# Kernel tuning notes

Hardware: AMD Instinct MI355X
Metric: run time of the kernel (lower is better)

The kernel has to match this reference:

```python
import jax, jax.numpy as jnp
import numpy as np

B, S, D, H, E, K, F = 1, 1024, 1024, 16, 8, 2, 4096


def setup_inputs() -> dict:
    key = jax.random.key(0)
    ks = jax.random.split(key, 8)
    n = lambda k, shape, sc: (jax.random.normal(k, shape, dtype=jnp.float32) * sc)
    return {
        "x": n(ks[0], (B, S, D), 1.0),
        "w_qkv": n(ks[1], (D, 3 * D), D ** -0.5),
        "w_o": n(ks[2], (D, D), D ** -0.5),
        "g1": jnp.ones((D,), jnp.float32),
        "b1": jnp.zeros((D,), jnp.float32),
        "wg": n(ks[3], (D, E), D ** -0.5),
        "w1": n(ks[4], (E, D, F), D ** -0.5),
        "bb1": jnp.zeros((E, F), jnp.float32),
        "w2": n(ks[5], (E, F, D), F ** -0.5),
        "bb2": jnp.zeros((E, D), jnp.float32),
        "g2": jnp.ones((D,), jnp.float32),
        "b2": jnp.zeros((D,), jnp.float32),
    }


def layernorm(x, g, b, eps=1e-5):
    m = x.mean(-1, keepdims=True)
    v = ((x - m) ** 2).mean(-1, keepdims=True)
    return (x - m) * jax.lax.rsqrt(v + eps) * g + b


def reference(x, w_qkv, w_o, g1, b1, wg, w1, bb1, w2, bb2, g2, b2):
    b, s, d = x.shape
    hd = d // H
    # --- multi-head causal self-attention ---
    qkv = x @ w_qkv  # [b,s,3d]
    q, k, v = jnp.split(qkv, 3, axis=-1)
    to_heads = lambda t: t.reshape(b, s, H, hd).transpose(0, 2, 1, 3)  # [b,h,s,hd]
    q, k, v = to_heads(q), to_heads(k), to_heads(v)
    scores = jnp.einsum("bhqd,bhkd->bhqk", q, k) / jnp.sqrt(jnp.float32(hd))
    causal = jnp.tril(jnp.ones((s, s), bool))
    scores = jnp.where(causal, scores, jnp.finfo(scores.dtype).min)
    attn = jax.nn.softmax(scores, axis=-1)
    o = jnp.einsum("bhqk,bhkd->bhqd", attn, v)
    o = o.transpose(0, 2, 1, 3).reshape(b, s, d) @ w_o
    # --- add & norm ---
    h = layernorm(x + o, g1, b1)
    # --- MoE FFN: softmax router, top-k, renormalized combine ---
    probs = jax.nn.softmax(h @ wg, axis=-1)  # [b,s,E]
    topv, topi = jax.lax.top_k(probs, K)
    topv = topv / topv.sum(-1, keepdims=True)
    w = (topv[..., None] * jax.nn.one_hot(topi, E, dtype=h.dtype)).sum(-2)  # [b,s,E]
    h1 = jax.nn.gelu(jnp.einsum("bsd,edf->ebsf", h, w1) + bb1[:, None, None, :])
    y = jnp.einsum("ebsf,efd->ebsd", h1, w2) + bb2[:, None, None, :]
    moe = jnp.einsum("ebsd,bse->bsd", y, w)
    # --- residual + norm of MoE block ---
    return layernorm(h + moe, g2, b2)
```

## Files before the change

kernel.cpp:

```cpp
#include <hip/hip_runtime.h>
#include <hip/hip_bf16.h>
#include <math.h>

#define SEQ 1024
#define DIM 1024
#define NH  16
#define NE  8
#define FF  4096
#define NCH 8

typedef float f32x4 __attribute__((ext_vector_type(4)));
typedef float f32x2 __attribute__((ext_vector_type(2)));
typedef short short8 __attribute__((ext_vector_type(8)));
typedef short s16x4 __attribute__((ext_vector_type(4)));

#define WAIT_VM(N) asm volatile("s_waitcnt vmcnt(" #N ")" ::: "memory")

__device__ __forceinline__ ushort f2bf(float f) {
  union { float f; unsigned u; } v; v.f = f;
  unsigned r = v.u + 0x7FFF + ((v.u >> 16) & 1);
  return (ushort)(r >> 16);
}
__device__ __forceinline__ float bf2f(ushort h) {
  union { unsigned u; float f; } v; v.u = ((unsigned)h) << 16;
  return v.f;
}

__device__ __forceinline__ float gelu_tanh(float x) {
  return 0.5f * x * (1.f + tanhf(0.7978845608028654f * (x + 0.044715f * x * x * x)));
}
__device__ __forceinline__ float gelu_fast(float x) {
  float u = 1.5957691216057308f * (x + 0.044715f * x * x * x);
  return x / (1.f + __expf(-u));
}

__device__ __forceinline__ void gl2lds16(const void* g, void* l) {
  __builtin_amdgcn_global_load_lds(
      (const __attribute__((address_space(1))) unsigned int*)g,
      (__attribute__((address_space(3))) unsigned int*)l, 16, 0, 0);
}

__global__ __launch_bounds__(256) void wconv_kernel(
    const float* __restrict__ wq, const float* __restrict__ wo,
    const float* __restrict__ x,
    ushort* __restrict__ wqT, ushort* __restrict__ wqTl,
    ushort* __restrict__ woT, ushort* __restrict__ woTl,
    ushort* __restrict__ xh, ushort* __restrict__ xl) {
  __shared__ __align__(16) ushort th[64 * 64];
  __shared__ __align__(16) ushort tl[64 * 64];
  int z = blockIdx.z, t = threadIdx.x;
  if (z == 2) {
    int blk = blockIdx.y * 64 + blockIdx.x;
    int i = (blk * 256 + t) * 4;
    f32x4 v = *(const f32x4*)&x[i];
    ushort h[4], l[4];
#pragma unroll
    for (int j = 0; j < 4; j++) { h[j] = f2bf(v[j]); l[j] = f2bf(v[j] - bf2f(h[j])); }
    *(s16x4*)&xh[i] = *(const s16x4*)h;
    *(s16x4*)&xl[i] = *(const s16x4*)l;
    return;
  }
  const float* src; ushort* dh; ushort* dl; int R, C, r0, c0;
  if (z == 0) {
    if (blockIdx.x >= 48) return;
    src = wq; dh = wqT; dl = wqTl;
    R = DIM; C = 3 * DIM; r0 = blockIdx.y * 64; c0 = blockIdx.x * 64;
  } else {
    if (blockIdx.x >= 16) return;
    src = wo; dh = woT; dl = woTl;
    R = DIM; C = DIM; r0 = blockIdx.y * 64; c0 = blockIdx.x * 64;
  }
  int ry = (t >> 4) * 4;
  int cx = (t & 15) * 4;
  f32x4 v[4];
#pragma unroll
  for (int j = 0; j < 4; j++)
    v[j] = *(const f32x4*)&src[(size_t)(r0 + ry + j) * C + c0 + cx];
#pragma unroll
  for (int i = 0; i < 4; i++) {
    int trow = cx + i;
    int o = trow * 64 + (((ry >> 3) ^ (trow & 7)) << 3) + (ry & 7);
    ushort uh[4], ul[4];
#pragma unroll
    for (int j = 0; j < 4; j++) {
      float f = v[j][i];
      ushort hh = f2bf(f);
      uh[j] = hh;
      ul[j] = f2bf(f - bf2f(hh));
    }
    *(s16x4*)&th[o] = *(const s16x4*)uh;
    *(s16x4*)&tl[o] = *(const s16x4*)ul;
  }
  __syncthreads();
  int tr = t >> 2, tc = (t & 3) * 16;
  int b0 = (tc >> 3) ^ (tr & 7);
  int b1 = ((tc >> 3) + 1) ^ (tr & 7);
  size_t dbase = (size_t)(c0 + tr) * R + r0 + tc;
  short8 u0 = *(const short8*)&th[tr * 64 + b0 * 8];
  short8 u1 = *(const short8*)&th[tr * 64 + b1 * 8];
  *(short8*)&dh[dbase] = u0;
  *(short8*)&dh[dbase + 8] = u1;
  short8 l0 = *(const short8*)&tl[tr * 64 + b0 * 8];
  short8 l1 = *(const short8*)&tl[tr * 64 + b1 * 8];
  *(short8*)&dl[dbase] = l0;
  *(short8*)&dl[dbase + 8] = l1;
}

__global__ __launch_bounds__(256) void bfsplit_kernel(const float* __restrict__ in,
                                                      ushort* __restrict__ oh,
                                                      ushort* __restrict__ ol) {
  int i = (blockIdx.x * 256 + threadIdx.x) * 4;
  f32x4 v = *(const f32x4*)&in[i];
  ushort h[4], l[4];
#pragma unroll
  for (int j = 0; j < 4; j++) { h[j] = f2bf(v[j]); l[j] = f2bf(v[j] - bf2f(h[j])); }
  *(s16x4*)&oh[i] = *(const s16x4*)h;
  *(s16x4*)&ol[i] = *(const s16x4*)l;
}

#define MM_FEXP_LOAD(ra0v, ra1v, rb0v, rb1v, rb2v, rb3v, T)            \
  { int _ko = (T) * 32;                                                \
    ra0v = *(const short8*)(aG[0] + _ko);                              \
    ra1v = *(const short8*)(aG[1] + _ko);                              \
    rb0v = *(const f32x4*)(bG + (size_t)(_ko + 0) * N);                \
    rb1v = *(const f32x4*)(bG + (size_t)(_ko + 1) * N);                \
    rb2v = *(const f32x4*)(bG + (size_t)(_ko + 2) * N);                \
    rb3v = *(const f32x4*)(bG + (size_t)(_ko + 3) * N); }

#define MM_FEXP_STAGE(buf, ra0v, ra1v, rb0v, rb1v, rb2v, rb3v)         \
  { *(short8*)&As[buf][aw[0]] = ra0v;                                  \
    *(short8*)&As[buf][aw[1]] = ra1v;                                  \
    _Pragma("unroll")                                                  \
    for (int i = 0; i < 4; i++) {                                      \
      ushort u[4];                                                     \
      u[0] = f2bf(rb0v[i]); u[1] = f2bf(rb1v[i]);                      \
      u[2] = f2bf(rb2v[i]); u[3] = f2bf(rb3v[i]);                      \
      *(s16x4*)&Bs[buf][(nb * 4 + i) * 40 + bslot * 4] = *(const s16x4*)u; } }

#define MM_FEXP_MFMA(buf)                                              \
  { short8 af[4], bf[4];                                               \
    _Pragma("unroll")                                                  \
    for (int mi = 0; mi < 4; mi++) af[mi] = *(const short8*)&As[buf][aro[mi]]; \
    _Pragma("unroll")                                                  \
    for (int ni = 0; ni < 4; ni++) bf[ni] = *(const short8*)&Bs[buf][bro[ni]]; \
    _Pragma("unroll")                                                  \
    for (int mi = 0; mi < 4; mi++)                                     \
      _Pragma("unroll")                                                \
      for (int ni = 0; ni < 4; ni++)                                   \
        acc[mi][ni] = __builtin_amdgcn_mfma_f32_16x16x32_bf16(af[mi], bf[ni], acc[mi][ni], 0, 0, 0); }

template <int EPI, int KSPLIT>
__global__ __launch_bounds__(256) void mm_fexp(
    const ushort* __restrict__ A, const float* __restrict__ Bf,
    const float* __restrict__ bias, void* __restrict__ Cout,
    const int* __restrict__ tok, const int* __restrict__ offcnt,
    int N, int K)
{
  int zz = blockIdx.z;
  int e  = (KSPLIT > 1) ? (zz & (NE - 1)) : zz;
  int ks = (KSPLIT > 1) ? (zz >> 3) : 0;
  int off = offcnt[e], cnt = offcnt[NE + e];
  int m0 = blockIdx.y * 128;
  if (m0 >= cnt) return;
  int n0 = blockIdx.x * 128;
  const float* Bp = Bf + (size_t)e * K * N;
  const int Kc = K / KSPLIT, kbase = ks * Kc;

  __shared__ __align__(16) ushort As[2][128 * 32];
  __shared__ __align__(16) ushort Bs[2][128 * 40];

  int t = threadIdx.x, lane = t & 63, w = t >> 6, wr = w >> 1, wc = w & 1;

  const ushort* aG[2]; int aw[2];
#pragma unroll
  for (int c = 0; c < 2; c++) {
    int gid = w * 128 + c * 64 + lane;
    int m = gid >> 2, p = gid & 3;
    int kg = p ^ ((m >> 1) & 3);
    int mc = m0 + m; if (mc > cnt - 1) mc = cnt - 1;
    int arow = tok ? tok[off + mc] : (off + mc);
    aG[c] = A + (size_t)arow * K + kbase + kg * 8;
    aw[c] = gid * 8;
  }

  int kb = t >> 5, nb = t & 31;
  const float* bG = Bp + (size_t)(kbase + kb * 4) * N + n0 + nb * 4;
  int bslot = kb ^ ((nb & 3) << 1);

  int aro[4], bro[4];
#pragma unroll
  for (int mi = 0; mi < 4; mi++) {
    int m = wr * 64 + mi * 16 + (lane & 15);
    aro[mi] = (m * 4 + ((lane >> 4) ^ ((m >> 1) & 3))) * 8;
  }
#pragma unroll
  for (int ni = 0; ni < 4; ni++) {
    int n = wc * 64 + ni * 16 + (lane & 15);
    bro[ni] = n * 40 + ((((lane >> 4) * 2) ^ (((n >> 2) & 3) << 1))) * 4;
  }

  f32x4 acc[4][4] = {};
  const int nt = Kc / 32;

  short8 raA0, raA1, raB0, raB1;
  f32x4 rbA0, rbA1, rbA2, rbA3, rbB0, rbB1, rbB2, rbB3;
  MM_FEXP_LOAD(raA0, raA1, rbA0, rbA1, rbA2, rbA3, 0);
  MM_FEXP_LOAD(raB0, raB1, rbB0, rbB1, rbB2, rbB3, 1);

  for (int tt = 0; tt < nt; tt += 2) {
    MM_FEXP_STAGE(0, raA0, raA1, rbA0, rbA1, rbA2, rbA3);
    if (tt + 2 < nt) MM_FEXP_LOAD(raA0, raA1, rbA0, rbA1, rbA2, rbA3, tt + 2);
    asm volatile("s_waitcnt lgkmcnt(0)" ::: "memory");
    __builtin_amdgcn_sched_barrier(0);
    __builtin_amdgcn_s_barrier();
    MM_FEXP_MFMA(0);
    MM_FEXP_STAGE(1, raB0, raB1, rbB0, rbB1, rbB2, rbB3);
    if (tt + 3 < nt) MM_FEXP_LOAD(raB0, raB1, rbB0, rbB1, rbB2, rbB3, tt + 3);
    asm volatile("s_waitcnt lgkmcnt(0)" ::: "memory");
    __builtin_amdgcn_sched_barrier(0);
    __builtin_amdgcn_s_barrier();
    MM_FEXP_MFMA(1);
  }

  const float* biasp = (EPI == 3) ? nullptr : bias + (size_t)e * N;
  float* Cp = (float*)Cout + (size_t)ks * 2048 * N;
#pragma unroll
  for (int mi = 0; mi < 4; mi++) {
#pragma unroll
    for (int j = 0; j < 4; j++) {
      int grow = m0 + wr * 64 + mi * 16 + (lane >> 4) * 4 + j;
      if (grow >= cnt) continue;
      size_t rbase = (size_t)(off + grow) * N;
#pragma unroll
      for (int ni = 0; ni < 4; ni++) {
        int gcol = n0 + wc * 64 + ni * 16 + (lane & 15);
        float v = acc[mi][ni][j];
        if (EPI == 1) ((ushort*)Cout)[rbase + gcol] = f2bf(gelu_fast(v + biasp[gcol]));
        else          Cp[rbase + gcol] = v;
      }
    }
  }
}

#undef MM_FEXP_LOAD
#undef MM_FEXP_STAGE
#undef MM_FEXP_MFMA

__global__ __launch_bounds__(256) void mm_split(
    const ushort* __restrict__ Ah, const ushort* __restrict__ Al,
    const ushort* __restrict__ Bh, const ushort* __restrict__ Bl,
    float* __restrict__ C, int N, int K)
{
  int m0 = blockIdx.y * 128;
  int n0 = blockIdx.x * 128;

  __shared__ __align__(16) ushort Ahs[2][4096], Als[2][4096];
  __shared__ __align__(16) ushort Bhs[2][4096], Bls[2][4096];

  int t = threadIdx.x, lane = t & 63, w = t >> 6, wr = w >> 1, wc = w & 1;

  const ushort *aGh[2], *aGl[2], *bGh[2], *bGl[2];
  int lofs[2];
#pragma unroll
  for (int c = 0; c < 2; c++) {
    int gid = w * 128 + c * 64 + lane;
    int m = gid >> 2, p = gid & 3;
    int kg = p ^ ((m >> 1) & 3);
    aGh[c] = Ah + (size_t)(m0 + m) * K + kg * 8;
    aGl[c] = Al + (size_t)(m0 + m) * K + kg * 8;
    bGh[c] = Bh + (size_t)(n0 + m) * K + kg * 8;
    bGl[c] = Bl + (size_t)(n0 + m) * K + kg * 8;
    lofs[c] = (w * 128 + c * 64) * 8;
  }

  int aro[4], bro[4];
#pragma unroll
  for (int mi = 0; mi < 4; mi++) {
    int m = wr * 64 + mi * 16 + (lane & 15);
    aro[mi] = (m * 4 + ((lane >> 4) ^ ((m >> 1) & 3))) * 8;
  }
#pragma unroll
  for (int ni = 0; ni < 4; ni++) {
    int n = wc * 64 + ni * 16 + (lane & 15);
    bro[ni] = (n * 4 + ((lane >> 4) ^ ((n >> 1) & 3))) * 8;
  }

  f32x4 acc[4][4] = {};
  const int nt = K / 32;

#pragma unroll
  for (int c = 0; c < 2; c++) {
    gl2lds16(aGh[c], &Ahs[0][lofs[c]]); gl2lds16(aGl[c], &Als[0][lofs[c]]);
    gl2lds16(bGh[c], &Bhs[0][lofs[c]]); gl2lds16(bGl[c], &Bls[0][lofs[c]]);
  }
  if (nt > 1) {
#pragma unroll
    for (int c = 0; c < 2; c++) {
      gl2lds16(aGh[c] + 32, &Ahs[1][lofs[c]]); gl2lds16(aGl[c] + 32, &Als[1][lofs[c]]);
      gl2lds16(bGh[c] + 32, &Bhs[1][lofs[c]]); gl2lds16(bGl[c] + 32, &Bls[1][lofs[c]]);
    }
  }

  for (int tt = 0; tt < nt; tt++) {
    if (tt + 1 < nt) WAIT_VM(8); else WAIT_VM(0);
    __builtin_amdgcn_s_barrier();
    int b = tt & 1;
    short8 ah[4], al_[4], bh[4], bl_[4];
#pragma unroll
    for (int mi = 0; mi < 4; mi++) {
      ah[mi] = *(const short8*)&Ahs[b][aro[mi]];
      al_[mi] = *(const short8*)&Als[b][aro[mi]];
    }
#pragma unroll
    for (int ni = 0; ni < 4; ni++) {
      bh[ni] = *(const short8*)&Bhs[b][bro[ni]];
      bl_[ni] = *(const short8*)&Bls[b][bro[ni]];
    }
#pragma unroll
    for (int mi = 0; mi < 4; mi++)
#pragma unroll
      for (int ni = 0; ni < 4; ni++) {
        acc[mi][ni] = __builtin_amdgcn_mfma_f32_16x16x32_bf16(al_[mi], bh[ni], acc[mi][ni], 0, 0, 0);
        acc[mi][ni] = __builtin_amdgcn_mfma_f32_16x16x32_bf16(ah[mi], bl_[ni], acc[mi][ni], 0, 0, 0);
        acc[mi][ni] = __builtin_amdgcn_mfma_f32_16x16x32_bf16(ah[mi], bh[ni], acc[mi][ni], 0, 0, 0);
      }
    asm volatile("s_waitcnt lgkmcnt(0)" ::: "memory");
    __builtin_amdgcn_sched_barrier(0);
    __builtin_amdgcn_s_barrier();
    if (tt + 2 < nt) {
      int ko = (tt + 2) * 32;
#pragma unroll
      for (int c = 0; c < 2; c++) {
        gl2lds16(aGh[c] + ko, &Ahs[b][lofs[c]]); gl2lds16(aGl[c] + ko, &Als[b][lofs[c]]);
        gl2lds16(bGh[c] + ko, &Bhs[b][lofs[c]]); gl2lds16(bGl[c] + ko, &Bls[b][lofs[c]]);
      }
    }
  }

#pragma unroll
  for (int mi = 0; mi < 4; mi++)
#pragma unroll
    for (int j = 0; j < 4; j++) {
      int grow = m0 + wr * 64 + mi * 16 + (lane >> 4) * 4 + j;
      size_t rbase = (size_t)grow * N;
#pragma unroll
      for (int ni = 0; ni < 4; ni++) {
        int gcol = n0 + wc * 64 + ni * 16 + (lane & 15);
        C[rbase + gcol] = acc[mi][ni][j];
      }
    }
}

template <int EPI, int SPLIT>
__global__ __launch_bounds__(256) void mm_bf16(
    const float* __restrict__ A, const float* __restrict__ B,
    const float* __restrict__ bias, float* __restrict__ C,
    const int* __restrict__ tok, const int* __restrict__ offcnt,
    int M, int N, int K)
{
  int e = blockIdx.z;
  int off = 0, cnt = M;
  if (offcnt) { off = offcnt[e]; cnt = offcnt[NE + e]; }
  int m0 = blockIdx.y * 128;
  if (m0 >= cnt) return;
  const float* Bp = B + (size_t)e * K * N;
  const float* biasp = (EPI == 0) ? nullptr : bias + (size_t)e * N;
  int n0 = blockIdx.x * 128;

  __shared__ __align__(16) ushort As[(SPLIT + 1) * 128 * 32];
  __shared__ __align__(16) ushort Bs[(SPLIT + 1) * 128 * 32];

  int t = threadIdx.x;
  int lane = t & 63;
  int w = t >> 6, wr = w >> 1, wc = w & 1;

  const float* aptr[2];
  int aws[2];
  for (int i = 0; i < 2; i++) {
    int mr = i * 64 + (t >> 2);
    int mc = m0 + mr; if (mc > cnt - 1) mc = cnt - 1;
    int arow = tok ? tok[off + mc] : (off + mc);
    aptr[i] = A + (size_t)arow * K + (t & 3) * 8;
    aws[i] = mr * 32 + (t & 3) * 8;
  }

  int bn = t >> 1, bkh = (t & 1) * 16;
  const float* bptr = Bp + (size_t)bkh * N + n0 + bn;
  int bws0 = bn * 32 + 8 * (((bkh >> 3) + 0) ^ (bn & 3));
  int bws1 = bn * 32 + 8 * (((bkh >> 3) + 1) ^ (bn & 3));

  int aro[4], bro[4];
#pragma unroll
  for (int mi = 0; mi < 4; mi++)
    aro[mi] = (wr * 64 + mi * 16 + (lane & 15)) * 32 + (lane >> 4) * 8;
#pragma unroll
  for (int ni = 0; ni < 4; ni++) {
    int n = wc * 64 + ni * 16 + (lane & 15);
    bro[ni] = n * 32 + 8 * ((lane >> 4) ^ (n & 3));
  }

  f32x4 acc[4][4] = {};

  for (int k0 = 0; k0 < K; k0 += 32) {
#pragma unroll
    for (int i = 0; i < 2; i++) {
      f32x4 v0 = *(const f32x4*)(aptr[i] + k0);
      f32x4 v1 = *(const f32x4*)(aptr[i] + k0 + 4);
      ushort uh[8], ul[8];
#pragma unroll
      for (int j = 0; j < 4; j++) {
        float f0 = v0[j], f1 = v1[j];
        ushort h0 = f2bf(f0), h1 = f2bf(f1);
        uh[j] = h0; uh[4 + j] = h1;
        if (SPLIT) { ul[j] = f2bf(f0 - bf2f(h0)); ul[4 + j] = f2bf(f1 - bf2f(h1)); }
      }
      *(short8*)&As[aws[i]] = *(const short8*)uh;
      if (SPLIT) *(short8*)&As[4096 + aws[i]] = *(const short8*)ul;
    }
    {
      const float* bp = bptr + (size_t)k0 * N;
      ushort uh[16], ul[16];
#pragma unroll
      for (int i = 0; i < 16; i++) {
        float f = bp[(size_t)i * N];
        ushort h = f2bf(f);
        uh[i] = h;
        if (SPLIT) ul[i] = f2bf(f - bf2f(h));
      }
      *(short8*)&Bs[bws0] = *(const short8*)&uh[0];
      *(short8*)&Bs[bws1] = *(const short8*)&uh[8];
      if (SPLIT) {
        *(short8*)&Bs[4096 + bws0] = *(const short8*)&ul[0];
        *(short8*)&Bs[4096 + bws1] = *(const short8*)&ul[8];
      }
    }
    __syncthreads();
    short8 afh[4], bfh[4], afl[4], bfl[4];
#pragma unroll
    for (int mi = 0; mi < 4; mi++) {
      afh[mi] = *(const short8*)&As[aro[mi]];
      if (SPLIT) afl[mi] = *(const short8*)&As[4096 + aro[mi]];
    }
#pragma unroll
    for (int ni = 0; ni < 4; ni++) {
      bfh[ni] = *(const short8*)&Bs[bro[ni]];
      if (SPLIT) bfl[ni] = *(const short8*)&Bs[4096 + bro[ni]];
    }
#pragma unroll
    for (int mi = 0; mi < 4; mi++)
#pragma unroll
      for (int ni = 0; ni < 4; ni++) {
        if (SPLIT) {
          acc[mi][ni] = __builtin_amdgcn_mfma_f32_16x16x32_bf16(afl[mi], bfh[ni], acc[mi][ni], 0, 0, 0);
          acc[mi][ni] = __builtin_amdgcn_mfma_f32_16x16x32_bf16(afh[mi], bfl[ni], acc[mi][ni], 0, 0, 0);
        }
        acc[mi][ni] = __builtin_amdgcn_mfma_f32_16x16x32_bf16(afh[mi], bfh[ni], acc[mi][ni], 0, 0, 0);
      }
    __syncthreads();
  }

#pragma unroll
  for (int mi = 0; mi < 4; mi++) {
#pragma unroll
    for (int j = 0; j < 4; j++) {
      int grow = m0 + wr * 64 + mi * 16 + (lane >> 4) * 4 + j;
      if (grow >= cnt) continue;
      size_t rbase = (size_t)(off + grow) * N;
#pragma unroll
      for (int ni = 0; ni < 4; ni++) {
        int gcol = n0 + wc * 64 + ni * 16 + (lane & 15);
        float v = acc[mi][ni][j];
        if (EPI >= 1) v += biasp[gcol];
        if (EPI == 1) v = gelu_tanh(v);
        C[rbase + gcol] = v;
      }
    }
  }
}

__device__ __forceinline__ int vidx(int d, int key) {
  return d * 64 + ((((key >> 3) ^ (d & 7)) << 3) | (key & 7));
}

__global__ __launch_bounds__(256, 1) void attn_mfma(const float* __restrict__ qkv,
                                                    float* __restrict__ opart,
                                                    float* __restrict__ ml) {
  const int qb = blockIdx.x;
  const int ch = blockIdx.y;
  const int head = blockIdx.z;
  const int q0 = qb * 128;
  const int t = threadIdx.x;
  const int lane = t & 63, w = t >> 6;
  const int g = lane >> 4, l4 = lane & 15;

  __shared__ __align__(16) ushort Kh[64 * 64], Kl[64 * 64];
  __shared__ __align__(16) ushort Vh[64 * 64], Vl[64 * 64];
  __shared__ __align__(16) ushort Ph[4][32 * 72], Pl[4][32 * 72];

  short8 qh[2][2], ql[2][2];
#pragma unroll
  for (int mi = 0; mi < 2; mi++)
#pragma unroll
    for (int ks = 0; ks < 2; ks++) {
      int row = q0 + w * 32 + mi * 16 + l4;
      const float* qp = qkv + (size_t)row * 3072 + head * 64 + ks * 32 + g * 8;
      f32x4 a = *(const f32x4*)qp;
      f32x4 b4 = *(const f32x4*)(qp + 4);
      ushort uh[8], ul_[8];
#pragma unroll
      for (int j = 0; j < 4; j++) {
        ushort h0 = f2bf(a[j]), h1 = f2bf(b4[j]);
        uh[j] = h0; uh[4 + j] = h1;
        ul_[j] = f2bf(a[j] - bf2f(h0)); ul_[4 + j] = f2bf(b4[j] - bf2f(h1));
      }
      qh[mi][ks] = *(const short8*)uh;
      ql[mi][ks] = *(const short8*)ul_;
    }

  float m_s[2][4], l_s[2][4];
  f32x4 O[2][4] = {};
#pragma unroll
  for (int mi = 0; mi < 2; mi++)
#pragma unroll
    for (int j = 0; j < 4; j++) { m_s[mi][j] = -1e30f; l_s[mi][j] = 0.f; }

  const int ntot = 2 * (qb + 1);
  const int kt_beg = (ch * ntot) / NCH;
  const int kt_end = ((ch + 1) * ntot) / NCH;
  for (int kt = kt_beg; kt < kt_end; kt++) {
    const int kv0 = kt * 64;
    __syncthreads();
    {
      int key = t >> 2;
      int dblk = (t & 3) * 16;
      const float* kp = qkv + (size_t)(kv0 + key) * 3072 + 1024 + head * 64 + dblk;
      const float* vp = kp + 1024;
      f32x4 k0 = *(const f32x4*)kp, k1 = *(const f32x4*)(kp + 4),
            k2 = *(const f32x4*)(kp + 8), k3 = *(const f32x4*)(kp + 12);
      f32x4 v0 = *(const f32x4*)vp, v1 = *(const f32x4*)(vp + 4),
            v2 = *(const f32x4*)(vp + 8), v3 = *(const f32x4*)(vp + 12);
      float kf[16] = {k0[0],k0[1],k0[2],k0[3], k1[0],k1[1],k1[2],k1[3],
                      k2[0],k2[1],k2[2],k2[3], k3[0],k3[1],k3[2],k3[3]};
      float vf[16] = {v0[0],v0[1],v0[2],v0[3], v1[0],v1[1],v1[2],v1[3],
                      v2[0],v2[1],v2[2],v2[3], v3[0],v3[1],v3[2],v3[3]};
#pragma unroll
      for (int half = 0; half < 2; half++) {
        int d8 = (dblk >> 3) + half;
        int idx = key * 64 + ((d8 ^ (key & 7)) << 3);
        ushort uh[8], ul_[8];
#pragma unroll
        for (int j = 0; j < 8; j++) {
          float f = kf[half * 8 + j];
          ushort h = f2bf(f);
          uh[j] = h; ul_[j] = f2bf(f - bf2f(h));
        }
        *(short8*)&Kh[idx] = *(const short8*)uh;
        *(short8*)&Kl[idx] = *(const short8*)ul_;
      }
#pragma unroll
      for (int i = 0; i < 16; i++) {
        int d = dblk + i;
        int idx = vidx(d, key);
        float f = vf[i];
        ushort h = f2bf(f);
        Vh[idx] = h; Vl[idx] = f2bf(f - bf2f(h));
      }
    }
    __syncthreads();

    if (kv0 <= q0 + w * 32 + 31) {
      f32x4 S[2][4] = {};
#pragma unroll
      for (int ks = 0; ks < 2; ks++) {
        short8 kbh[4], kbl[4];
#pragma unroll
        for (int ni = 0; ni < 4; ni++) {
          int key = ni * 16 + l4;
          int d8 = ks * 4 + g;
          int idx = key * 64 + ((d8 ^ (key & 7)) << 3);
          kbh[ni] = *(const short8*)&Kh[idx];
          kbl[ni] = *(const short8*)&Kl[idx];
        }
#pragma unroll
        for (int mi = 0; mi < 2; mi++)
#pragma unroll
          for (int ni = 0; ni < 4; ni++) {
            S[mi][ni] = __builtin_amdgcn_mfma_f32_16x16x32_bf16(ql[mi][ks], kbh[ni], S[mi][ni], 0, 0, 0);
            S[mi][ni] = __builtin_amdgcn_mfma_f32_16x16x32_bf16(qh[mi][ks], kbl[ni], S[mi][ni], 0, 0, 0);
            S[mi][ni] = __builtin_amdgcn_mfma_f32_16x16x32_bf16(qh[mi][ks], kbh[ni], S[mi][ni], 0, 0, 0);
          }
      }
#pragma unroll
      for (int mi = 0; mi < 2; mi++) {
        int rowb = q0 + w * 32 + mi * 16 + g * 4;
        float mx[4] = {-1e30f, -1e30f, -1e30f, -1e30f};
#pragma unroll
        for (int ni = 0; ni < 4; ni++) {
          int col = kv0 + ni * 16 + l4;
#pragma unroll
          for (int j = 0; j < 4; j++) {
            float s = S[mi][ni][j] * 0.125f;
            if (col > rowb + j) s = -1e30f;
            S[mi][ni][j] = s;
            mx[j] = fmaxf(mx[j], s);
          }
        }
#pragma unroll
        for (int j = 0; j < 4; j++) {
#pragma unroll
          for (int msk = 8; msk; msk >>= 1) mx[j] = fmaxf(mx[j], __shfl_xor(mx[j], msk));
          float mn = fmaxf(m_s[mi][j], mx[j]);
          float sc = __expf(m_s[mi][j] - mn);
          m_s[mi][j] = mn;
          l_s[mi][j] *= sc;
#pragma unroll
          for (int df = 0; df < 4; df++) O[mi][df][j] *= sc;
        }
        float ps[4] = {0.f, 0.f, 0.f, 0.f};
#pragma unroll
        for (int ni = 0; ni < 4; ni++)
#pragma unroll
          for (int j = 0; j < 4; j++) {
            float p = __expf(S[mi][ni][j] - m_s[mi][j]);
            ps[j] += p;
            int rl = mi * 16 + g * 4 + j, cl = ni * 16 + l4;
            ushort h = f2bf(p);
            Ph[w][rl * 72 + cl] = h;
            Pl[w][rl * 72 + cl] = f2bf(p - bf2f(h));
          }
#pragma unroll
        for (int j = 0; j < 4; j++) {
#pragma unroll
          for (int msk = 8; msk; msk >>= 1) ps[j] += __shfl_xor(ps[j], msk);
          l_s[mi][j] += ps[j];
        }
      }
      asm volatile("s_waitcnt lgkmcnt(0)" ::: "memory");
      __builtin_amdgcn_sched_barrier(0);
#pragma unroll
      for (int ks = 0; ks < 2; ks++) {
        short8 pah[2], pal[2], vbh[4], vbl[4];
#pragma unroll
        for (int mi = 0; mi < 2; mi++) {
          int idx = (mi * 16 + l4) * 72 + ks * 32 + g * 8;
          pah[mi] = *(const short8*)&Ph[w][idx];
          pal[mi] = *(const short8*)&Pl[w][idx];
        }
#pragma unroll
        for (int df = 0; df < 4; df++) {
          int d = df * 16 + l4;
          int k8 = ks * 4 + g;
          int idx = d * 64 + ((k8 ^ (d & 7)) << 3);
          vbh[df] = *(const short8*)&Vh[idx];
          vbl[df] = *(const short8*)&Vl[idx];
        }
#pragma unroll
        for (int mi = 0; mi < 2; mi++)
#pragma unroll
          for (int df = 0; df < 4; df++) {
            O[mi][df] = __builtin_amdgcn_mfma_f32_16x16x32_bf16(pal[mi], vbh[df], O[mi][df], 0, 0, 0);
            O[mi][df] = __builtin_amdgcn_mfma_f32_16x16x32_bf16(pah[mi], vbl[df], O[mi][df], 0, 0, 0);
            O[mi][df] = __builtin_amdgcn_mfma_f32_16x16x32_bf16(pah[mi], vbh[df], O[mi][df], 0, 0, 0);
          }
      }
    }
  }

#pragma unroll
  for (int mi = 0; mi < 2; mi++)
#pragma unroll
    for (int j = 0; j < 4; j++) {
      int row = q0 + w * 32 + mi * 16 + g * 4 + j;
      if (l4 == 0) {
        float* mlp = ml + (((size_t)ch * NH + head) * SEQ + row) * 2;
        mlp[0] = m_s[mi][j];
        mlp[1] = l_s[mi][j];
      }
#pragma unroll
      for (int df = 0; df < 4; df++)
        opart[(size_t)ch * (SEQ * DIM) + (size_t)row * DIM + head * 64 + df * 16 + l4] =
            O[mi][df][j];
    }
}

template <int SPLIT>
__global__ __launch_bounds__(256) void attn_combine(const float* __restrict__ opart,
                                                    const float* __restrict__ ml,
                                                    float* __restrict__ o,
                                                    ushort* __restrict__ oh,
                                                    ushort* __restrict__ ol) {
  int row = blockIdx.x, t = threadIdx.x;
  int d0 = t * 4;
  int head = d0 >> 6;
  float m[NCH], l[NCH];
#pragma unroll
  for (int ch = 0; ch < NCH; ch++) {
    const float* p = ml + (((size_t)ch * NH + head) * SEQ + row) * 2;
    m[ch] = p[0]; l[ch] = p[1];
  }
  float M = m[0];
#pragma unroll
  for (int ch = 1; ch < NCH; ch++) M = fmaxf(M, m[ch]);
  float wgt[NCH], den = 0.f;
#pragma unroll
  for (int ch = 0; ch < NCH; ch++) { wgt[ch] = __expf(m[ch] - M); den += l[ch] * wgt[ch]; }
  float inv = 1.f / den;
  f32x4 r = {0.f, 0.f, 0.f, 0.f};
#pragma unroll
  for (int ch = 0; ch < NCH; ch++) {
    f32x4 O = *(const f32x4*)&opart[(size_t)ch * (SEQ * DIM) + (size_t)row * DIM + d0];
#pragma unroll
    for (int j = 0; j < 4; j++) r[j] += O[j] * wgt[ch];
  }
#pragma unroll
  for (int j = 0; j < 4; j++) r[j] *= inv;
  if (SPLIT) {
    ushort hh[4], ll[4];
#pragma unroll
    for (int j = 0; j < 4; j++) { hh[j] = f2bf(r[j]); ll[j] = f2bf(r[j] - bf2f(hh[j])); }
    *(s16x4*)&oh[(size_t)row * DIM + d0] = *(const s16x4*)hh;
    *(s16x4*)&ol[(size_t)row * DIM + d0] = *(const s16x4*)ll;
  } else {
    *(f32x4*)&o[(size_t)row * DIM + d0] = r;
  }
}

__device__ float block_reduce_256(float v, float* red, int t) {
  red[t] = v; __syncthreads();
  for (int st = 128; st > 0; st >>= 1) {
    if (t < st) red[t] += red[t + st];
    __syncthreads();
  }
  float r = red[0];
  __syncthreads();
  return r;
}

__global__ __launch_bounds__(256) void addln_router_kernel(
    const float* __restrict__ x, const float* __restrict__ r,
    const float* __restrict__ g, const float* __restrict__ b,
    const float* __restrict__ wg,
    float* __restrict__ out, ushort* __restrict__ outb,
    int* __restrict__ topi, float* __restrict__ topw) {
  __shared__ float red[256];
  __shared__ float red2[NE][256];
  int row = blockIdx.x, t = threadIdx.x;
  float vals[4];
  float s = 0.f;
  for (int i = 0; i < 4; i++) {
    int d = t + i * 256;
    vals[i] = x[(size_t)row * DIM + d] + r[(size_t)row * DIM + d];
    s += vals[i];
  }
  float mean = block_reduce_256(s, red, t) * (1.f / DIM);
  float vs = 0.f;
  for (int i = 0; i < 4; i++) { float d = vals[i] - mean; vs += d * d; }
  float var = block_reduce_256(vs, red, t) * (1.f / DIM);
  float inv = rsqrtf(var + 1e-5f);
  float hv4[4];
  for (int i = 0; i < 4; i++) {
    int d = t + i * 256;
    float v = (vals[i] - mean) * inv * g[d] + b[d];
    hv4[i] = v;
    out[(size_t)row * DIM + d] = v;
    outb[(size_t)row * DIM + d] = f2bf(v);
  }
  float acc[NE] = {};
  for (int i = 0; i < 4; i++) {
    int d = t + i * 256;
    const float* wr = wg + (size_t)d * NE;
    for (int e = 0; e < NE; e++) acc[e] += hv4[i] * wr[e];
  }
  for (int e = 0; e < NE; e++) red2[e][t] = acc[e];
  __syncthreads();
  for (int st = 128; st > 0; st >>= 1) {
    if (t < st)
      for (int e = 0; e < NE; e++) red2[e][t] += red2[e][t + st];
    __syncthreads();
  }
  if (t == 0) {
    float l[NE];
    for (int e = 0; e < NE; e++) l[e] = red2[e][0];
    int i0 = 0;
    for (int e = 1; e < NE; e++) if (l[e] > l[i0]) i0 = e;
    int i1 = -1;
    for (int e = 0; e < NE; e++) {
      if (e == i0) continue;
      if (i1 < 0 || l[e] > l[i1]) i1 = e;
    }
    float p1 = __expf(l[i1] - l[i0]);
    float iv = 1.f / (1.f + p1);
    topi[row * 2] = i0; topi[row * 2 + 1] = i1;
    topw[row * 2] = iv; topw[row * 2 + 1] = p1 * iv;
  }
}

__global__ __launch_bounds__(256) void addln_kernel(const float* __restrict__ x,
                                                    const float* __restrict__ r,
                                                    const float* __restrict__ g,
                                                    const float* __restrict__ b,
                                                    float* __restrict__ out,
                                                    ushort* __restrict__ outb) {
  __shared__ float red[256];
  int row = blockIdx.x, t = threadIdx.x;
  float vals[4];
  float s = 0.f;
  for (int i = 0; i < 4; i++) {
    int d = t + i * 256;
    vals[i] = x[(size_t)row * DIM + d] + r[(size_t)row * DIM + d];
    s += vals[i];
  }
  float mean = block_reduce_256(s, red, t) * (1.f / DIM);
  float vs = 0.f;
  for (int i = 0; i < 4; i++) { float d = vals[i] - mean; vs += d * d; }
  float var = block_reduce_256(vs, red, t) * (1.f / DIM);
  float inv = rsqrtf(var + 1e-5f);
  for (int i = 0; i < 4; i++) {
    int d = t + i * 256;
    float v = (vals[i] - mean) * inv * g[d] + b[d];
    out[(size_t)row * DIM + d] = v;
    if (outb) outb[(size_t)row * DIM + d] = f2bf(v);
  }
}

__global__ __launch_bounds__(256) void router_kernel(const float* __restrict__ h,
                                                     const float* __restrict__ wg,
                                                     int* __restrict__ topi,
                                                     float* __restrict__ topw) {
  __shared__ float red[NE][256];
  int tkn = blockIdx.x, t = threadIdx.x;
  float acc[NE] = {};
  for (int i = 0; i < 4; i++) {
    int d = t + i * 256;
    float hv = h[(size_t)tkn * DIM + d];
    const float* wr = wg + (size_t)d * NE;
    for (int e = 0; e < NE; e++) acc[e] += hv * wr[e];
  }
  for (int e = 0; e < NE; e++) red[e][t] = acc[e];
  __syncthreads();
  for (int st = 128; st > 0; st >>= 1) {
    if (t < st)
      for (int e = 0; e < NE; e++) red[e][t] += red[e][t + st];
    __syncthreads();
  }
  if (t == 0) {
    float l[NE];
    for (int e = 0; e < NE; e++) l[e] = red[e][0];
    int i0 = 0;
    for (int e = 1; e < NE; e++) if (l[e] > l[i0]) i0 = e;
    int i1 = -1;
    for (int e = 0; e < NE; e++) {
      if (e == i0) continue;
      if (i1 < 0 || l[e] > l[i1]) i1 = e;
    }
    float p1 = __expf(l[i1] - l[i0]);
    float inv = 1.f / (1.f + p1);
    topi[tkn * 2] = i0; topi[tkn * 2 + 1] = i1;
    topw[tkn * 2] = inv; topw[tkn * 2 + 1] = p1 * inv;
  }
}

__global__ __launch_bounds__(1024) void compact_kernel(const int* __restrict__ topi,
                                                       int* __restrict__ tok,
                                                       int* __restrict__ assign_row,
                                                       int* __restrict__ offcnt) {
  __shared__ int wsum[16];
  int t = threadIdx.x, lane = t & 63, w = t >> 6;
  int i0 = topi[t * 2], i1 = topi[t * 2 + 1];
  int base = 0;
  for (int e = 0; e < NE; e++) {
    int which = (i0 == e) ? 0 : ((i1 == e) ? 1 : -1);
    unsigned long long mask = __ballot(which >= 0);
    unsigned long long lem = (lane == 63) ? ~0ULL : ((1ULL << (lane + 1)) - 1ULL);
    int incl = __popcll(mask & lem);
    if (lane == 0) wsum[w] = __popcll(mask);
    __syncthreads();
    int pre = 0, tot = 0;
    for (int i = 0; i < 16; i++) { if (i < w) pre += wsum[i]; tot += wsum[i]; }
    if (which >= 0) {
      int pos = base + pre + incl - 1;
      tok[pos] = t;
      assign_row[t * 2 + which] = pos;
    }
    if (t == 0) { offcnt[e] = base; offcnt[NE + e] = tot; }
    base += tot;
    __syncthreads();
  }
}

template <int KS>
__global__ __launch_bounds__(256) void final_ln_kernel(const float* __restrict__ h,
                                                       const float* __restrict__ y,
                                                       const int* __restrict__ assign_row,
                                                       const float* __restrict__ topw,
                                                       const int* __restrict__ topi,
                                                       const float* __restrict__ bb2,
                                                       const float* __restrict__ g,
                                                       const float* __restrict__ b,
                                                       float* __restrict__ out) {
  __shared__ float red[256];
  int row = blockIdx.x, t = threadIdx.x;
  int r0 = assign_row[row * 2], r1 = assign_row[row * 2 + 1];
  float w0 = topw[row * 2], w1 = topw[row * 2 + 1];
  float vals[4];
  float s = 0.f;
  for (int i = 0; i < 4; i++) {
    int d = t + i * 256;
    float acc0 = 0.f, acc1 = 0.f;
#pragma unroll
    for (int p = 0; p < KS; p++) {
      acc0 += y[(size_t)p * 2048 * DIM + (size_t)r0 * DIM + d];
      acc1 += y[(size_t)p * 2048 * DIM + (size_t)r1 * DIM + d];
    }
    float v = h[(size_t)row * DIM + d] + w0 * acc0 + w1 * acc1;
    if (KS > 1) {
      int e0 = topi[row * 2], e1 = topi[row * 2 + 1];
      v += w0 * bb2[e0 * DIM + d] + w1 * bb2[e1 * DIM + d];
    }
    vals[i] = v;
    s += v;
  }
  float mean = block_reduce_256(s, red, t) * (1.f / DIM);
  float vs = 0.f;
  for (int i = 0; i < 4; i++) { float d = vals[i] - mean; vs += d * d; }
  float var = block_reduce_256(vs, red, t) * (1.f / DIM);
  float inv = rsqrtf(var + 1e-5f);
  for (int i = 0; i < 4; i++) {
    int d = t + i * 256;
    out[(size_t)row * DIM + d] = (vals[i] - mean) * inv * g[d] + b[d];
  }
}

extern "C" void kernel_launch(void* const* d_in, const int* in_sizes, int n_in,
                              void* d_out, int out_size, void* d_ws, size_t ws_size,
                              hipStream_t stream) {
  const float* x     = (const float*)d_in[0];
  const float* w_qkv = (const float*)d_in[1];
  const float* w_o   = (const float*)d_in[2];
  const float* g1    = (const float*)d_in[3];
  const float* b1    = (const float*)d_in[4];
  const float* wg    = (const float*)d_in[5];
  const float* w1    = (const float*)d_in[6];
  const float* bb1   = (const float*)d_in[7];
  const float* w2    = (const float*)d_in[8];
  const float* bb2   = (const float*)d_in[9];
  const float* g2    = (const float*)d_in[10];
  const float* b2    = (const float*)d_in[11];
  float* out = (float*)d_out;
  float* ws = (float*)d_ws;

  const bool fast = ws_size >= (size_t)46671872 * 4;

  if (fast) {
    float* qkv    = ws;
    float* oproj  = ws + 4194304;
    float* h      = ws + 5242880;
    float* ybuf   = ws + 6291456;
    float* topw   = ws + 8388608;
    int*   ibase  = (int*)(ws + 8390656);
    int* topi       = ibase;
    int* tok        = ibase + 2048;
    int* assign_row = ibase + 4096;
    int* offcnt     = ibase + 6144;
    ushort* hb  = (ushort*)(ws + 8398848);
    ushort* h1b = (ushort*)(ws + 8923136);
    ushort* wqT  = (ushort*)(ws + 13117440);
    ushort* wqTl = wqT + 3145728;
    ushort* woT  = wqT + 6291456;
    ushort* woTl = wqT + 7340032;
    float* ypart = ws + 17311744;
    float* mlbuf = ws + 25700352;
    ushort* xh = (ushort*)ybuf;
    ushort* xl = xh + 1048576;
    ushort* oh = xh + 2097152;
    ushort* ol = xh + 3145728;
    float* opart = ypart;

    wconv_kernel<<<dim3(64, 16, 3), 256, 0, stream>>>(w_qkv, w_o, x,
                                                      wqT, wqTl, woT, woTl, xh, xl);
    mm_split<<<dim3(24, 8), 256, 0, stream>>>(xh, xl, wqT, wqTl, qkv, 3 * DIM, DIM);
    attn_mfma<<<dim3(8, NCH, NH), 256, 0, stream>>>(qkv, opart, mlbuf);
    attn_combine<1><<<dim3(SEQ), 256, 0, stream>>>(opart, mlbuf, nullptr, oh, ol);
    mm_split<<<dim3(8, 8), 256, 0, stream>>>(oh, ol, woT, woTl, oproj, DIM, DIM);
    addln_router_kernel<<<dim3(SEQ), 256, 0, stream>>>(x, oproj, g1, b1, wg,
                                                       h, hb, topi, topw);
    compact_kernel<<<dim3(1), 1024, 0, stream>>>(topi, tok, assign_row, offcnt);
    mm_fexp<1, 1><<<dim3(FF / 128, 8, NE), 256, 0, stream>>>(hb, w1, bb1, (void*)h1b,
                                                             tok, offcnt, FF, DIM);
    mm_fexp<3, 4><<<dim3(DIM / 128, 8, NE * 4), 256, 0, stream>>>(h1b, w2, nullptr,
                                                                  (void*)ypart,
                                                                  nullptr, offcnt, DIM, FF);
    final_ln_kernel<4><<<dim3(SEQ), 256, 0, stream>>>(h, ypart, assign_row, topw,
                                                      topi, bb2, g2, b2, out);
  } else {
    float* qkv    = ws;
    float* attn_o = ws + 3145728;
    float* oproj  = ws + 4194304;
    float* h      = ws + 5242880;
    float* h1     = ws + 6291456;
    float* ybuf   = ws + 14680064;
    float* topw   = ws + 16777216;
    int*   ibase  = (int*)(ws + 16779264);
    int* topi       = ibase;
    int* tok        = ibase + 2048;
    int* assign_row = ibase + 4096;
    int* offcnt     = ibase + 6144;
    float* opart = h1;
    float* mlbuf = ybuf;

    mm_bf16<0, 1><<<dim3(24, 8, 1), 256, 0, stream>>>(x, w_qkv, nullptr, qkv,
                                                      nullptr, nullptr, SEQ, 3 * DIM, DIM);
    attn_mfma<<<dim3(8, NCH, NH), 256, 0, stream>>>(qkv, opart, mlbuf);
    attn_combine<0><<<dim3(SEQ), 256, 0, stream>>>(opart, mlbuf, attn_o, nullptr, nullptr);
    mm_bf16<0, 1><<<dim3(8, 8, 1), 256, 0, stream>>>(attn_o, w_o, nullptr, oproj,
                                                     nullptr, nullptr, SEQ, DIM, DIM);
    addln_kernel<<<dim3(SEQ), 256, 0, stream>>>(x, oproj, g1, b1, h, nullptr);
    router_kernel<<<dim3(SEQ), 256, 0, stream>>>(h, wg, topi, topw);
    compact_kernel<<<dim3(1), 1024, 0, stream>>>(topi, tok, assign_row, offcnt);
    mm_bf16<1, 0><<<dim3(32, 8, NE), 256, 0, stream>>>(h, w1, bb1, h1,
                                                       tok, offcnt, SEQ, FF, DIM);
    mm_bf16<2, 0><<<dim3(8, 8, NE), 256, 0, stream>>>(h1, w2, bb2, ybuf,
                                                      nullptr, offcnt, SEQ, DIM, FF);
    final_ln_kernel<1><<<dim3(SEQ), 256, 0, stream>>>(h, ybuf, assign_row, topw,
                                                      nullptr, nullptr, g2, b2, out);
  }
}
```

Before: 311.6 us.

## Restructure MoE expert GEMM into split-B-half pipeline with 1x4 warp layout

Reworks the fp32-weight expert GEMM: warps now tile 32 rows by all 128 columns instead of a 2x2 grid of 64x64, and each K-tile's B staging is split into two column halves. The second half is converted and stored while the MFMAs for the first half run, so fp32-to-bf16 conversion and global loads overlap with matrix math. Prefetch depth drops from two tiles to one, which frees registers but adds an extra barrier per K-tile and gives less latency hiding for the global loads.

After: 325.1 us. 4.3% more time.

```diff
diff --git a/kernel.cpp b/kernel.cpp
--- a/kernel.cpp
+++ b/kernel.cpp
@@ -117,37 +117,6 @@
   *(s16x4*)&oh[i] = *(const s16x4*)h;
   *(s16x4*)&ol[i] = *(const s16x4*)l;
 }
-
-#define MM_FEXP_LOAD(ra0v, ra1v, rb0v, rb1v, rb2v, rb3v, T)            \
-  { int _ko = (T) * 32;                                                \
-    ra0v = *(const short8*)(aG[0] + _ko);                              \
-    ra1v = *(const short8*)(aG[1] + _ko);                              \
-    rb0v = *(const f32x4*)(bG + (size_t)(_ko + 0) * N);                \
-    rb1v = *(const f32x4*)(bG + (size_t)(_ko + 1) * N);                \
-    rb2v = *(const f32x4*)(bG + (size_t)(_ko + 2) * N);                \
-    rb3v = *(const f32x4*)(bG + (size_t)(_ko + 3) * N); }
-
-#define MM_FEXP_STAGE(buf, ra0v, ra1v, rb0v, rb1v, rb2v, rb3v)         \
-  { *(short8*)&As[buf][aw[0]] = ra0v;                                  \
-    *(short8*)&As[buf][aw[1]] = ra1v;                                  \
-    _Pragma("unroll")                                                  \
-    for (int i = 0; i < 4; i++) {                                      \
-      ushort u[4];                                                     \
-      u[0] = f2bf(rb0v[i]); u[1] = f2bf(rb1v[i]);                      \
-      u[2] = f2bf(rb2v[i]); u[3] = f2bf(rb3v[i]);                      \
-      *(s16x4*)&Bs[buf][(nb * 4 + i) * 40 + bslot * 4] = *(const s16x4*)u; } }
-
-#define MM_FEXP_MFMA(buf)                                              \
-  { short8 af[4], bf[4];                                               \
-    _Pragma("unroll")                                                  \
-    for (int mi = 0; mi < 4; mi++) af[mi] = *(const short8*)&As[buf][aro[mi]]; \
-    _Pragma("unroll")                                                  \
-    for (int ni = 0; ni < 4; ni++) bf[ni] = *(const short8*)&Bs[buf][bro[ni]]; \
-    _Pragma("unroll")                                                  \
-    for (int mi = 0; mi < 4; mi++)                                     \
-      _Pragma("unroll")                                                \
-      for (int ni = 0; ni < 4; ni++)                                   \
-        acc[mi][ni] = __builtin_amdgcn_mfma_f32_16x16x32_bf16(af[mi], bf[ni], acc[mi][ni], 0, 0, 0); }
 
 template <int EPI, int KSPLIT>
 __global__ __launch_bounds__(256) void mm_fexp(
@@ -169,7 +138,8 @@
   __shared__ __align__(16) ushort As[2][128 * 32];
   __shared__ __align__(16) ushort Bs[2][128 * 40];
 
-  int t = threadIdx.x, lane = t & 63, w = t >> 6, wr = w >> 1, wc = w & 1;
+  int t = threadIdx.x, lane = t & 63, w = t >> 6;
+  int g = lane >> 4, l4 = lane & 15;
 
   const ushort* aG[2]; int aw[2];
 #pragma unroll
@@ -183,57 +153,120 @@
     aw[c] = gid * 8;
   }
 
-  int kb = t >> 5, nb = t & 31;
-  const float* bG = Bp + (size_t)(kbase + kb * 4) * N + n0 + nb * 4;
-  int bslot = kb ^ ((nb & 3) << 1);
-
-  int aro[4], bro[4];
-#pragma unroll
-  for (int mi = 0; mi < 4; mi++) {
-    int m = wr * 64 + mi * 16 + (lane & 15);
-    aro[mi] = (m * 4 + ((lane >> 4) ^ ((m >> 1) & 3))) * 8;
-  }
-#pragma unroll
-  for (int ni = 0; ni < 4; ni++) {
-    int n = wc * 64 + ni * 16 + (lane & 15);
-    bro[ni] = n * 40 + ((((lane >> 4) * 2) ^ (((n >> 2) & 3) << 1))) * 4;
-  }
-
-  f32x4 acc[4][4] = {};
+  int kb = t >> 5, nbp = t & 31;
+  const float* bG0 = Bp + (size_t)(kbase + kb * 4) * N + n0 + nbp * 2;
+  const float* bG1 = bG0 + 64;
+  int col0 = nbp * 2, col1 = 64 + nbp * 2;
+  int bs0 = kb ^ (((col0 >> 2) & 3) << 1);
+  int bs1 = kb ^ (((col1 >> 2) & 3) << 1);
+
+  int aro[2], bro[8];
+#pragma unroll
+  for (int mi = 0; mi < 2; mi++) {
+    int m = w * 32 + mi * 16 + l4;
+    aro[mi] = (m * 4 + (g ^ ((m >> 1) & 3))) * 8;
+  }
+#pragma unroll
+  for (int ni = 0; ni < 8; ni++) {
+    int n = ni * 16 + l4;
+    bro[ni] = n * 40 + ((g * 2) ^ (((n >> 2) & 3) << 1)) * 4;
+  }
+
+  f32x4 acc[2][8] = {};
   const int nt = Kc / 32;
 
-  short8 raA0, raA1, raB0, raB1;
-  f32x4 rbA0, rbA1, rbA2, rbA3, rbB0, rbB1, rbB2, rbB3;
-  MM_FEXP_LOAD(raA0, raA1, rbA0, rbA1, rbA2, rbA3, 0);
-  MM_FEXP_LOAD(raB0, raB1, rbB0, rbB1, rbB2, rbB3, 1);
-
-  for (int tt = 0; tt < nt; tt += 2) {
-    MM_FEXP_STAGE(0, raA0, raA1, rbA0, rbA1, rbA2, rbA3);
-    if (tt + 2 < nt) MM_FEXP_LOAD(raA0, raA1, rbA0, rbA1, rbA2, rbA3, tt + 2);
+  short8 rA0, rA1;
+  f32x2 rb00, rb01, rb02, rb03;
+  f32x2 rb10, rb11, rb12, rb13;
+
+#define FEXP_LDA(T) { int _ko = (T) * 32;                                \
+    rA0 = *(const short8*)(aG[0] + _ko);                                 \
+    rA1 = *(const short8*)(aG[1] + _ko); }
+#define FEXP_LDB0(T) { int _ko = (T) * 32;                               \
+    rb00 = *(const f32x2*)(bG0 + (size_t)(_ko + 0) * N);                 \
+    rb01 = *(const f32x2*)(bG0 + (size_t)(_ko + 1) * N);                 \
+    rb02 = *(const f32x2*)(bG0 + (size_t)(_ko + 2) * N);                 \
+    rb03 = *(const f32x2*)(bG0 + (size_t)(_ko + 3) * N); }
+#define FEXP_LDB1(T) { int _ko = (T) * 32;                               \
+    rb10 = *(const f32x2*)(bG1 + (size_t)(_ko + 0) * N);                 \
+    rb11 = *(const f32x2*)(bG1 + (size_t)(_ko + 1) * N);                 \
+    rb12 = *(const f32x2*)(bG1 + (size_t)(_ko + 2) * N);                 \
+    rb13 = *(const f32x2*)(bG1 + (size_t)(_ko + 3) * N); }
+
+  FEXP_LDA(0); FEXP_LDB0(0); FEXP_LDB1(0);
+
+  for (int tt = 0; tt < nt; tt++) {
+    int buf = tt & 1;
+    *(short8*)&As[buf][aw[0]] = rA0;
+    *(short8*)&As[buf][aw[1]] = rA1;
+    {
+      ushort ua[4] = { f2bf(rb00[0]), f2bf(rb01[0]), f2bf(rb02[0]), f2bf(rb03[0]) };
+      ushort ub[4] = { f2bf(rb00[1]), f2bf(rb01[1]), f2bf(rb02[1]), f2bf(rb03[1]) };
+      *(s16x4*)&Bs[buf][col0 * 40 + bs0 * 4] = *(const s16x4*)ua;
+      *(s16x4*)&Bs[buf][(col0 + 1) * 40 + bs0 * 4] = *(const s16x4*)ub;
+    }
+    if (tt + 1 < nt) { FEXP_LDA(tt + 1); FEXP_LDB0(tt + 1); }
     asm volatile("s_waitcnt lgkmcnt(0)" ::: "memory");
     __builtin_amdgcn_sched_barrier(0);
     __builtin_amdgcn_s_barrier();
-    MM_FEXP_MFMA(0);
-    MM_FEXP_STAGE(1, raB0, raB1, rbB0, rbB1, rbB2, rbB3);
-    if (tt + 3 < nt) MM_FEXP_LOAD(raB0, raB1, rbB0, rbB1, rbB2, rbB3, tt + 3);
+    short8 af0 = *(const short8*)&As[buf][aro[0]];
+    short8 af1 = *(const short8*)&As[buf][aro[1]];
+    {
+      short8 b0 = *(const short8*)&Bs[buf][bro[0]];
+      short8 b1 = *(const short8*)&Bs[buf][bro[1]];
+      short8 b2 = *(const short8*)&Bs[buf][bro[2]];
+      short8 b3 = *(const short8*)&Bs[buf][bro[3]];
+      acc[0][0] = __builtin_amdgcn_mfma_f32_16x16x32_bf16(af0, b0, acc[0][0], 0, 0, 0);
+      acc[0][1] = __builtin_amdgcn_mfma_f32_16x16x32_bf16(af0, b1, acc[0][1], 0, 0, 0);
+      acc[0][2] = __builtin_amdgcn_mfma_f32_16x16x32_bf16(af0, b2, acc[0][2], 0, 0, 0);
+      acc[0][3] = __builtin_amdgcn_mfma_f32_16x16x32_bf16(af0, b3, acc[0][3], 0, 0, 0);
+      acc[1][0] = __builtin_amdgcn_mfma_f32_16x16x32_bf16(af1, b0, acc[1][0], 0, 0, 0);
+      acc[1][1] = __builtin_amdgcn_mfma_f32_16x16x32_bf16(af1, b1, acc[1][1], 0, 0, 0);
+      acc[1][2] = __builtin_amdgcn_mfma_f32_16x16x32_bf16(af1, b2, acc[1][2], 0, 0, 0);
+      acc[1][3] = __builtin_amdgcn_mfma_f32_16x16x32_bf16(af1, b3, acc[1][3], 0, 0, 0);
+    }
+    {
+      ushort ua[4] = { f2bf(rb10[0]), f2bf(rb11[0]), f2bf(rb12[0]), f2bf(rb13[0]) };
+      ushort ub[4] = { f2bf(rb10[1]), f2bf(rb11[1]), f2bf(rb12[1]), f2bf(rb13[1]) };
+      *(s16x4*)&Bs[buf][col1 * 40 + bs1 * 4] = *(const s16x4*)ua;
+      *(s16x4*)&Bs[buf][(col1 + 1) * 40 + bs1 * 4] = *(const s16x4*)ub;
+    }
+    if (tt + 1 < nt) FEXP_LDB1(tt + 1);
     asm volatile("s_waitcnt lgkmcnt(0)" ::: "memory");
     __builtin_amdgcn_sched_barrier(0);
     __builtin_amdgcn_s_barrier();
-    MM_FEXP_MFMA(1);
-  }
+    {
+      short8 b4 = *(const short8*)&Bs[buf][bro[4]];
+      short8 b5 = *(const short8*)&Bs[buf][bro[5]];
+      short8 b6 = *(const short8*)&Bs[buf][bro[6]];
+      short8 b7 = *(const short8*)&Bs[buf][bro[7]];
+      acc[0][4] = __builtin_amdgcn_mfma_f32_16x16x32_bf16(af0, b4, acc[0][4], 0, 0, 0);
+      acc[0][5] = __builtin_amdgcn_mfma_f32_16x16x32_bf16(af0, b5, acc[0][5], 0, 0, 0);
+      acc[0][6] = __builtin_amdgcn_mfma_f32_16x16x32_bf16(af0, b6, acc[0][6], 0, 0, 0);
+      acc[0][7] = __builtin_amdgcn_mfma_f32_16x16x32_bf16(af0, b7, acc[0][7], 0, 0, 0);
+      acc[1][4] = __builtin_amdgcn_mfma_f32_16x16x32_bf16(af1, b4, acc[1][4], 0, 0, 0);
+      acc[1][5] = __builtin_amdgcn_mfma_f32_16x16x32_bf16(af1, b5, acc[1][5], 0, 0, 0);
+      acc[1][6] = __builtin_amdgcn_mfma_f32_16x16x32_bf16(af1, b6, acc[1][6], 0, 0, 0);
+      acc[1][7] = __builtin_amdgcn_mfma_f32_16x16x32_bf16(af1, b7, acc[1][7], 0, 0, 0);
+    }
+  }
+
+#undef FEXP_LDA
+#undef FEXP_LDB0
+#undef FEXP_LDB1
 
   const float* biasp = (EPI == 3) ? nullptr : bias + (size_t)e * N;
   float* Cp = (float*)Cout + (size_t)ks * 2048 * N;
 #pragma unroll
-  for (int mi = 0; mi < 4; mi++) {
+  for (int mi = 0; mi < 2; mi++) {
 #pragma unroll
     for (int j = 0; j < 4; j++) {
-      int grow = m0 + wr * 64 + mi * 16 + (lane >> 4) * 4 + j;
+      int grow = m0 + w * 32 + mi * 16 + g * 4 + j;
       if (grow >= cnt) continue;
       size_t rbase = (size_t)(off + grow) * N;
 #pragma unroll
-      for (int ni = 0; ni < 4; ni++) {
-        int gcol = n0 + wc * 64 + ni * 16 + (lane & 15);
+      for (int ni = 0; ni < 8; ni++) {
+        int gcol = n0 + ni * 16 + l4;
         float v = acc[mi][ni][j];
         if (EPI == 1) ((ushort*)Cout)[rbase + gcol] = f2bf(gelu_fast(v + biasp[gcol]));
         else          Cp[rbase + gcol] = v;
@@ -241,10 +274,6 @@
     }
   }
 }
-
-#undef MM_FEXP_LOAD
-#undef MM_FEXP_STAGE
-#undef MM_FEXP_MFMA
 
 __global__ __launch_bounds__(256) void mm_split(
     const ushort* __restrict__ Ah, const ushort* __restrict__ Al,
```
